# Kernel tuning notes

Hardware: AMD Instinct MI355X
Metric: run time of the kernel (lower is better)

Reference implementation:

```python
import jax, jax.numpy as jnp
import numpy as np
from jax import lax

K = 5          # dynamic kernel size
GROUPS = 8     # inter_channels // group_channels = 128 // 16
R = 2          # pixel shuffle upscale factor
SLOPE = 0.01   # LeakyReLU default negative_slope
EPS = 1e-5     # BatchNorm eps


def conv2d(x, w, b, pad=0):
    # x: [B,C,H,W], w: [O,I,kh,kw]
    y = lax.conv_general_dilated(x, w, (1, 1), [(pad, pad), (pad, pad)],
                                 dimension_numbers=('NCHW', 'OIHW', 'NCHW'))
    return y + b[None, :, None, None]


def pixel_shuffle(x, r):
    B, C, H, W = x.shape
    x = x.reshape(B, C // (r * r), r, r, H, W)
    x = x.transpose(0, 1, 4, 2, 5, 3)  # B, C', H, r, W, r
    return x.reshape(B, C // (r * r), H * r, W * r)


def involution(x, weight, k, groups, pad):
    # x: [B,C,H,W]; weight: [B,groups,k,k,H,W]
    # out[b, g*gc+c, h, w] = sum_ij weight[b,g,i,j,h,w] * x_pad[b, g*gc+c, h+i, w+j]
    B, C, H, W = x.shape
    gc = C // groups
    xp = jnp.pad(x, ((0, 0), (0, 0), (pad, pad), (pad, pad)))
    xg = xp.reshape(B, groups, gc, H + 2 * pad, W + 2 * pad)
    out = jnp.zeros((B, groups, gc, H, W), x.dtype)
    for i in range(k):
        for j in range(k):
            out = out + weight[:, :, None, i, j] * xg[:, :, :, i:i + H, j:j + W]
    return out.reshape(B, C, H, W)


def setup_inputs() -> dict:
    key = jax.random.key(0)
    ks = jax.random.split(key, 16)
    s = 0.05
    return {
        'high_level': jax.random.normal(ks[0], (8, 128, 64, 64), jnp.float32),
        'low_level': jax.random.normal(ks[1], (8, 224, 128, 128), jnp.float32),
        'emb': jax.random.normal(ks[2], (8, 256, 128, 128), jnp.float32),
        'reduce_w': jax.random.normal(ks[3], (128, 256, 1, 1), jnp.float32) * s,
        'reduce_b': jax.random.normal(ks[4], (128,), jnp.float32) * s,
        'conv1_w': jax.random.normal(ks[5], (32, 128, 1, 1), jnp.float32) * s,
        'conv1_b': jax.random.normal(ks[6], (32,), jnp.float32) * s,
        'conv2_w': jax.random.normal(ks[7], (200, 32, 3, 3), jnp.float32) * s,
        'conv2_b': jax.random.normal(ks[8], (200,), jnp.float32) * s,
        'embconv_w': jax.random.normal(ks[9], (32, 256, 1, 1), jnp.float32) * s,
        'embconv_b': jax.random.normal(ks[10], (32,), jnp.float32) * s,
        'out_w': jax.random.normal(ks[11], (64, 128, 1, 1), jnp.float32) * s,
        'out_b': jax.random.normal(ks[12], (64,), jnp.float32) * s,
        'bn_gamma': jnp.ones((64,), jnp.float32),
        'bn_beta': jnp.zeros((64,), jnp.float32),
        'bn_mean': jnp.zeros((64,), jnp.float32),
        'bn_var': jax.random.uniform(ks[13], (64,), jnp.float32, 0.5, 1.5),
    }


def reference(high_level, low_level, emb,
              reduce_w, reduce_b, conv1_w, conv1_b, conv2_w, conv2_b,
              embconv_w, embconv_b, out_w, out_b,
              bn_gamma, bn_beta, bn_mean, bn_var):
    cat = jnp.concatenate([pixel_shuffle(high_level, R), low_level], axis=1)
    cat = conv2d(cat, reduce_w, reduce_b)
    mix = jax.nn.leaky_relu(conv2d(cat, conv1_w, conv1_b)
                            + conv2d(emb, embconv_w, embconv_b), SLOPE)
    w = conv2d(mix, conv2_w, conv2_b, pad=1)  # [B, K*K*GROUPS, H, W]
    B, _, H, W = w.shape
    w = w.reshape(B, GROUPS, K, K, H, W)
    o = involution(cat, w, K, GROUPS, (K - 1) // 2)
    o = conv2d(o, out_w, out_b)
    o = (o - bn_mean[None, :, None, None]) * (bn_gamma[None, :, None, None]
        / jnp.sqrt(bn_var[None, :, None, None] + EPS)) + bn_beta[None, :, None, None]
    return jax.nn.leaky_relu(o, SLOPE)
```

## Files before the change

kernel.cpp:

```cpp
#include <hip/hip_runtime.h>

typedef unsigned short u16; typedef unsigned int u32; typedef unsigned long long u64;
typedef __attribute__((ext_vector_type(8))) short short8;
typedef __attribute__((ext_vector_type(16))) float f32x16;

#define HW 16384

#define RED_B  0
#define C1E_B  128
#define C2_B   160
#define OUT_B  416
#define BN_SC  480
#define BN_SH  544
#define FLAG_OFF   4096
#define RWB_OFF    8192
#define C1B_OFF    73728
#define EMBB_OFF   81920
#define OUTB_OFF   98304
#define C2PB_OFF   114688
#define WEFF_OFF   262144
#define CAT2_OFF   524288
#define MIX_OFF    34078720

__device__ __forceinline__ float bf2f(u16 x){ u32 u=((u32)x)<<16; float f; __builtin_memcpy(&f,&u,4); return f; }
__device__ __forceinline__ u16 f2bf(float f){ u32 u; __builtin_memcpy(&u,&f,4); return (u16)((u + 0x7fffu + ((u>>16)&1u))>>16); }
__device__ __forceinline__ u32 pk2(float a, float b){ return (u32)f2bf(a) | ((u32)f2bf(b)<<16); }
__device__ __forceinline__ float lrelu(float x){ return x>0.f ? x : 0.01f*x; }

template<int M> __device__ __forceinline__ u16 ldb(const void* p, size_t i){
    if (M==1) return ((const u16*)p)[i];
    return f2bf(((const float*)p)[i]);
}
template<int M> __device__ __forceinline__ float ldf(const void* p, size_t i){
    if (M==1) return bf2f(((const u16*)p)[i]);
    return ((const float*)p)[i];
}
__device__ __forceinline__ int swz(int p){ return ((p>>1) ^ (p>>3)) & 7; }

__device__ __forceinline__ void gl16(const void* g, void* l){
    __builtin_amdgcn_global_load_lds(
        (const __attribute__((address_space(1))) u32*)g,
        (__attribute__((address_space(3))) u32*)l, 16, 0, 0);
}

__global__ void detect_kernel(const void* __restrict__ emb, u32* __restrict__ flag){
    int tid = threadIdx.x;
    const u16* p = (const u16*)emb;
    int e = (p[tid*2] >> 7) & 0xFF;
    u64 m = __ballot(e >= 100 && e <= 140);
    if (tid == 0) *flag = (__popcll(m) >= 32) ? 1u : 0u;
}

template<int M>
__device__ __forceinline__ void prep_body(
    const void* rw, const void* rb, const void* c1w, const void* c1b,
    const void* c2w, const void* c2b, const void* ew, const void* eb,
    const void* ow, const void* ob, const void* gam, const void* bet,
    const void* mn, const void* vr, char* ws)
{
    float* wf = (float*)ws;
    int i = blockIdx.x*256 + threadIdx.x;
    if (i < 32768) {
        int o = i>>8, ic = i&255;
        int s = ic>>4, qq = (ic>>3)&1, e = ic&7;
        int dst = (((o>>5)*16 + s)*64 + qq*32 + (o&31))*8 + e;
        ((u16*)(ws+RWB_OFF))[dst] = ldb<M>(rw, i);
    }
    else if (i < 36864)  ((u16*)(ws+C1B_OFF))[i-32768] = ldb<M>(c1w, i-32768);
    else if (i < 45056)  ((u16*)(ws+EMBB_OFF))[i-36864] = ldb<M>(ew, i-36864);
    else if (i < 53248)  ((u16*)(ws+OUTB_OFF))[i-45056] = ldb<M>(ow, i-45056);
    else if (i < 126976) {
        int j = i-53248; int o = j/288, k = j - o*288;
        int tap = k>>5, ic = k&31;
        u16 v = 0;
        if (o < 200) v = ldb<M>(c2w, (size_t)o*288 + ic*9 + tap);
        ((u16*)(ws+C2PB_OFF))[j] = v;
    }
    else if (i < 127584) {
        int j = i-126976;
        if (j < 128) wf[RED_B+j] = ldf<M>(rb, j);
        else if (j < 160) {
            int o = j-128;
            float s = ldf<M>(c1b,o) + ldf<M>(eb,o);
#pragma unroll 8
            for (int ic=0; ic<128; ic++)
                s += ldf<M>(c1w, (size_t)o*128+ic) * ldf<M>(rb, ic);
            wf[C1E_B+o] = s;
        }
        else if (j < 416) { int o = j-160; wf[C2_B+o] = (o<200) ? ldf<M>(c2b,o) : 0.f; }
        else if (j < 480) wf[OUT_B+j-416] = ldf<M>(ob, j-416);
        else if (j < 544) { int c=j-480; wf[BN_SC+c] = ldf<M>(gam,c) * rsqrtf(ldf<M>(vr,c)+1e-5f); }
        else { int c=j-544; wf[BN_SH+c] = ldf<M>(bet,c) - ldf<M>(mn,c)*ldf<M>(gam,c)*rsqrtf(ldf<M>(vr,c)+1e-5f); }
    }
    else if (i < 135776) {
        int j = i - 127584; int oc = j>>8, k2 = j&255;
        float s = 0.f;
#pragma unroll 8
        for (int ic=0; ic<128; ic++)
            s += ldf<M>(c1w, (size_t)oc*128+ic) * ldf<M>(rw, (size_t)ic*256+k2);
        ((u16*)(ws+WEFF_OFF))[oc*256+k2] = f2bf(s);
    }
}

__global__ __launch_bounds__(256) void k_prep(
    const void* rw, const void* rb, const void* c1w, const void* c1b,
    const void* c2w, const void* c2b, const void* ew, const void* eb,
    const void* ow, const void* ob, const void* gam, const void* bet,
    const void* mn, const void* vr, char* ws, const u32* __restrict__ flag)
{
    if (*flag) prep_body<1>(rw,rb,c1w,c1b,c2w,c2b,ew,eb,ow,ob,gam,bet,mn,vr,ws);
    else       prep_body<0>(rw,rb,c1w,c1b,c2w,c2b,ew,eb,ow,ob,gam,bet,mn,vr,ws);
}

__device__ __forceinline__ void trans_half_f32(
    const float* rowbase, int rstart, int po, int jh, u16* At, int chunkIdx)
{
    u32 R2[4][4];
#pragma unroll
    for (int jp=0;jp<4;jp++){
        int r = rstart + 4*jh + jp;
        int v = (r>>2)&15;
        float fa[4], fb[4];
        __builtin_memcpy(fa, rowbase + r*64 + ((2*po)^v)*4, 16);
        __builtin_memcpy(fb, rowbase + r*64 + ((2*po+1)^v)*4, 16);
        R2[jp][0]=pk2(fa[0],fa[1]); R2[jp][1]=pk2(fa[2],fa[3]);
        R2[jp][2]=pk2(fb[0],fb[1]); R2[jp][3]=pk2(fb[2],fb[3]);
    }
#pragma unroll
    for (int p=0;p<8;p++){
        const int u=p>>1, hf=p&1;
        u32 Wh[2];
#pragma unroll
        for (int mp=0;mp<2;mp++){
            u32 A0=R2[2*mp][u], A1=R2[2*mp+1][u];
            Wh[mp] = hf ? ((A0>>16)|(A1&0xffff0000u)) : ((A0&0xffffu)|(A1<<16));
        }
        int pg = 8*po+p;
        __builtin_memcpy(At + pg*264 + ((chunkIdx ^ swz(pg))<<3) + jh*4, Wh, 8);
    }
}

__global__ __launch_bounds__(512) void k_rmf(
    const void* __restrict__ hi, const void* __restrict__ lo, const void* __restrict__ emb,
    const u16* __restrict__ rwB, const u16* __restrict__ weffB, const u16* __restrict__ embB,
    const float* __restrict__ wf, u16* __restrict__ cat2, u16* __restrict__ mixt,
    const u32* __restrict__ flag)
{
    if (*flag != 0u) return;
    __shared__ float rawf[18432];
    __shared__ u16 At[64*264];

    const int tid = threadIdx.x, wvi = tid>>6, lane = tid&63;
    const int col = lane&31, q = lane>>5;
    const int gpx = blockIdx.x*64;
    const int b = gpx>>14, p0 = gpx&16383;
    const int h = p0>>7, w0 = p0&127;

    for (int i=wvi; i<56; i+=8){
        int r = 4*i + (lane>>4);
        int qd = (lane&15) ^ (i&15);
        gl16((const float*)lo + ((size_t)(b*224 + r))*HW + p0 + qd*4,
             (char*)rawf + i*1024);
    }
    for (int i=wvi; i<16; i+=8){
        int hc = 8*i + (lane>>3);
        int qd = (lane&7) ^ (i&7);
        gl16((const float*)hi + ((size_t)(b*128 + hc))*4096 + (size_t)(h>>1)*64 + (w0>>1) + qd*4,
             (char*)rawf + 57344 + i*1024);
    }
    __syncthreads();

    {
        const int co = tid>>4, po = (tid>>1)&7, jh = tid&1;
        if (co >= 4) {
            trans_half_f32(rawf, 8*(co-4), po, jh, At, co);
        } else {
            const int h2 = (h&1)*2;
            u32 E2[4][2], O2[4][2];
#pragma unroll
            for (int jp=0;jp<4;jp++){
                int hc = (8*co + 4*jh + jp)*4 + h2;
                int slot = po ^ ((hc>>3)&7);
                float fe[4], fo[4];
                __builtin_memcpy(fe, rawf + 14336 + hc*32 + slot*4, 16);
                __builtin_memcpy(fo, rawf + 14336 + (hc+1)*32 + slot*4, 16);
                E2[jp][0]=pk2(fe[0],fe[1]); E2[jp][1]=pk2(fe[2],fe[3]);
                O2[jp][0]=pk2(fo[0],fo[1]); O2[jp][1]=pk2(fo[2],fo[3]);
            }
#pragma unroll
            for (int p=0;p<8;p++){
                const int k=p>>1, u=k>>1, hf=k&1;
                u32 Wh[2];
#pragma unroll
                for (int mp=0;mp<2;mp++){
                    u32 A0 = (p&1) ? O2[2*mp][u] : E2[2*mp][u];
                    u32 A1 = (p&1) ? O2[2*mp+1][u] : E2[2*mp+1][u];
                    Wh[mp] = hf ? ((A0>>16)|(A1&0xffff0000u)) : ((A0&0xffffu)|(A1<<16));
                }
                int pg = 8*po+p;
                __builtin_memcpy(At + pg*264 + ((co ^ swz(pg))<<3) + jh*4, Wh, 8);
            }
        }
    }
    __syncthreads();

    for (int i=wvi; i<64; i+=8){
        int r = 4*i + (lane>>4);
        int qd = (lane&15) ^ (i&15);
        gl16((const float*)emb + ((size_t)(b*256 + r))*HW + p0 + qd*4,
             (char*)rawf + i*1024);
    }

    const int pt = wvi>>2, ks = wvi&3;
    const int pp = pt*32 + col, sw = swz(pp);
    const u16* arow = At + pp*264;

    f32x16 racc, macc;
#pragma unroll
    for (int r=0;r<16;r++){ racc[r]=0.f; macc[r]=0.f; }

    short8 Wf[4];
#pragma unroll
    for (int t4=0;t4<4;t4++)
        __builtin_memcpy(&Wf[t4], weffB + (size_t)col*256 + (4*ks+t4)*16 + q*8, 16);

#pragma unroll
    for (int bt=0; bt<4; bt++){
        short8 Bb[4];
#pragma unroll
        for (int si=0;si<4;si++)
            __builtin_memcpy(&Bb[si], rwB + (((size_t)(ks*16 + bt*4 + si))*64 + lane)*8, 16);
#pragma unroll
        for (int si=0;si<4;si++){
            int s = bt*4 + si;
            short8 a; __builtin_memcpy(&a, arow + (((2*s+q)^sw)<<3), 16);
            racc = __builtin_amdgcn_mfma_f32_32x32x16_bf16(a, Bb[si], racc, 0,0,0);
            int d = s - 4*ks;
            if (d>=0 && d<4)
                macc = __builtin_amdgcn_mfma_f32_32x32x16_bf16(a, Wf[d], macc, 0,0,0);
        }
    }
    {
        int oc = ks*32 + col;
        float bias = wf[RED_B + oc];
#pragma unroll
        for (int r=0;r<16;r++){
            int row = (r&3) + 8*(r>>2) + 4*q;
            cat2[((size_t)(gpx + pt*32 + row))*128 + oc] = f2bf(racc[r] + bias);
        }
    }
    __syncthreads();

    {
        const int co = tid>>4, po = (tid>>1)&7, jh = tid&1;
        trans_half_f32(rawf, 8*co, po, jh, At, co);
    }
    __syncthreads();

    {
        short8 Be[4];
#pragma unroll
        for (int t4=0;t4<4;t4++)
            __builtin_memcpy(&Be[t4], embB + (size_t)col*256 + (4*ks+t4)*16 + q*8, 16);
#pragma unroll
        for (int t4=0;t4<4;t4++){
            int t = 4*ks + t4;
            short8 a; __builtin_memcpy(&a, arow + (((2*t+q)^sw)<<3), 16);
            macc = __builtin_amdgcn_mfma_f32_32x32x16_bf16(a, Be[t4], macc, 0,0,0);
        }
    }

    float* exch = rawf;
    if (ks != 0){
#pragma unroll
        for (int r=0;r<16;r++){
            int row = (r&3) + 8*(r>>2) + 4*q;
            exch[pt*3072 + (ks-1)*1024 + row*32 + col] = macc[r];
        }
    }
    __syncthreads();
    if (ks == 0){
        float bias = wf[C1E_B + col];
#pragma unroll
        for (int r=0;r<16;r++){
            int row = (r&3) + 8*(r>>2) + 4*q;
            int base = pt*3072 + row*32 + col;
            float v = macc[r] + exch[base] + exch[base+1024] + exch[base+2048] + bias;
            mixt[((size_t)(gpx + pt*32 + row))*32 + col] = f2bf(lrelu(v));
        }
    }
}

__global__ __launch_bounds__(512) void k_rm(
    const void* __restrict__ hi, const void* __restrict__ lo, const void* __restrict__ emb,
    const u16* __restrict__ rwB, const u16* __restrict__ weffB, const u16* __restrict__ embB,
    const float* __restrict__ wf, u16* __restrict__ cat2, u16* __restrict__ mixt,
    const u32* __restrict__ flag)
{
    if (*flag != 1u) return;
    __shared__ u16 At1[64*264];
    __shared__ u16 At2[64*264];
    __shared__ u16 raw[34816];

    const int tid = threadIdx.x, wvi = tid>>6, lane = tid&63;
    const int col = lane&31, q = lane>>5;
    const int gpx = blockIdx.x*64;
    const int b = gpx>>14, p0 = gpx&16383;
    const int h = p0>>7, w0 = p0&127;

    {
        for (int i=wvi; i<28; i+=8){
            int chunk = i*64 + lane;
            int ch = chunk>>3, p8 = chunk&7;
            gl16((const u16*)lo + ((size_t)(b*224+ch))*HW + p0 + p8*8,
                 (char*)raw + i*1024);
        }
        {
            int i = wvi;
            int chunk = i*64 + lane;
            int hc = chunk>>2, c4 = chunk&3;
            gl16((const u16*)hi + ((size_t)(b*128+hc))*4096 + (size_t)(h>>1)*64 + (w0>>1) + c4*8,
                 (char*)raw + 28672 + i*1024);
        }
        for (int i=wvi; i<32; i+=8){
            int chunk = i*64 + lane;
            int ch = chunk>>3, p8 = chunk&7;
            gl16((const u16*)emb + ((size_t)(b*256+ch))*HW + p0 + p8*8,
                 (char*)raw + 36864 + i*1024);
        }
    }
    __syncthreads();

    {
        const int sthr = tid & 255;
        const int co = sthr>>3, po = sthr&7;
        u32 W[8][4];
        if (tid >= 256) {
            u32 R[8][4];
#pragma unroll
            for (int j=0;j<8;j++)
                __builtin_memcpy(&R[j][0], raw + 18432 + (8*co+j)*64 + po*8, 16);
#pragma unroll
            for (int p=0;p<8;p++){
                const int u = p>>1, hf = p&1;
#pragma unroll
                for (int m=0;m<4;m++){
                    u32 A0 = R[2*m][u], A1 = R[2*m+1][u];
                    W[p][m] = hf ? ((A0>>16) | (A1 & 0xffff0000u))
                                 : ((A0 & 0xffffu) | (A1<<16));
                }
            }
#pragma unroll
            for (int p=0;p<8;p++){
                int pg = 8*po + p;
                __builtin_memcpy(At2 + pg*264 + ((co ^ swz(pg))<<3), &W[p][0], 16);
            }
        } else if (co >= 4) {
            u32 R[8][4];
#pragma unroll
            for (int j=0;j<8;j++)
                __builtin_memcpy(&R[j][0], raw + (8*(co-4)+j)*64 + po*8, 16);
#pragma unroll
            for (int p=0;p<8;p++){
                const int u = p>>1, hf = p&1;
#pragma unroll
                for (int m=0;m<4;m++){
                    u32 A0 = R[2*m][u], A1 = R[2*m+1][u];
                    W[p][m] = hf ? ((A0>>16) | (A1 & 0xffff0000u))
                                 : ((A0 & 0xffffu) | (A1<<16));
                }
            }
#pragma unroll
            for (int p=0;p<8;p++){
                int pg = 8*po + p;
                __builtin_memcpy(At1 + pg*264 + ((co ^ swz(pg))<<3), &W[p][0], 16);
            }
        } else {
            const int h2 = (h&1)*2;
            u32 E[8][2], O[8][2];
#pragma unroll
            for (int j=0;j<8;j++){
                int hc = (8*co+j)*4 + h2;
                __builtin_memcpy(&E[j][0], raw + 14336 + hc*32 + po*4, 8);
                __builtin_memcpy(&O[j][0], raw + 14336 + (hc+1)*32 + po*4, 8);
            }
#pragma unroll
            for (int p=0;p<8;p++){
                const int k = p>>1, u = k>>1, hf = k&1;
#pragma unroll
                for (int m=0;m<4;m++){
                    u32 A0, A1;
                    if (p&1){ A0 = O[2*m][u]; A1 = O[2*m+1][u]; }
                    else    { A0 = E[2*m][u]; A1 = E[2*m+1][u]; }
                    W[p][m] = hf ? ((A0>>16) | (A1 & 0xffff0000u))
                                 : ((A0 & 0xffffu) | (A1<<16));
                }
            }
#pragma unroll
            for (int p=0;p<8;p++){
                int pg = 8*po + p;
                __builtin_memcpy(At1 + pg*264 + ((co ^ swz(pg))<<3), &W[p][0], 16);
            }
        }
    }
    __syncthreads();

    const int pt = wvi>>2, ks = wvi&3;
    const int pp = pt*32 + col, sw = swz(pp);
    const u16* arow1 = At1 + pp*264;
    const u16* arow2 = At2 + pp*264;

    f32x16 racc, macc;
#pragma unroll
    for (int r=0;r<16;r++){ racc[r]=0.f; macc[r]=0.f; }

    short8 Wf[4], Be2[4];
#pragma unroll
    for (int t4=0;t4<4;t4++)
        __builtin_memcpy(&Wf[t4], weffB + (size_t)col*256 + (4*ks+t4)*16 + q*8, 16);
#pragma unroll
    for (int t4=0;t4<4;t4++)
        __builtin_memcpy(&Be2[t4], embB + (size_t)col*256 + (4*ks+t4)*16 + q*8, 16);

#pragma unroll
    for (int bt=0; bt<4; bt++){
        short8 Bb[4];
#pragma unroll
        for (int si=0;si<4;si++)
            __builtin_memcpy(&Bb[si], rwB + (((size_t)(ks*16 + bt*4 + si))*64 + lane)*8, 16);
#pragma unroll
        for (int si=0;si<4;si++){
            int s = bt*4 + si;
            short8 a; __builtin_memcpy(&a, arow1 + (((2*s+q)^sw)<<3), 16);
            racc = __builtin_amdgcn_mfma_f32_32x32x16_bf16(a, Bb[si], racc, 0,0,0);
            int d = s - 4*ks;
            if (d>=0 && d<4)
                macc = __builtin_amdgcn_mfma_f32_32x32x16_bf16(a, Wf[d], macc, 0,0,0);
        }
    }
#pragma unroll
    for (int t4=0;t4<4;t4++){
        int t = 4*ks + t4;
        short8 a; __builtin_memcpy(&a, arow2 + (((2*t+q)^sw)<<3), 16);
        macc = __builtin_amdgcn_mfma_f32_32x32x16_bf16(a, Be2[t4], macc, 0,0,0);
    }
    {
        int oc = ks*32 + col;
        float bias = wf[RED_B + oc];
#pragma unroll
        for (int r=0;r<16;r++){
            int row = (r&3) + 8*(r>>2) + 4*q;
            cat2[((size_t)(gpx + pt*32 + row))*128 + oc] = f2bf(racc[r] + bias);
        }
    }

    float* exch = (float*)raw;
    if (ks != 0){
#pragma unroll
        for (int r=0;r<16;r++){
            int row = (r&3) + 8*(r>>2) + 4*q;
            exch[pt*3072 + (ks-1)*1024 + row*32 + col] = macc[r];
        }
    }
    __syncthreads();
    if (ks == 0){
        float bias = wf[C1E_B + col];
#pragma unroll
        for (int r=0;r<16;r++){
            int row = (r&3) + 8*(r>>2) + 4*q;
            int base = pt*3072 + row*32 + col;
            float v = macc[r] + exch[base] + exch[base+1024] + exch[base+2048] + bias;
            mixt[((size_t)(gpx + pt*32 + row))*32 + col] = f2bf(lrelu(v));
        }
    }
}

template<int M>
__device__ __forceinline__ void inv_body(
    const u16* __restrict__ cat2, const u16* __restrict__ mixt,
    const u16* __restrict__ c2B, const u16* __restrict__ outB,
    const float* __restrict__ wf, void* __restrict__ out,
    u16* halo_m, u16* wgt_l, u16* halo_c, u16* og)
{
    const int tid = threadIdx.x, wvi = tid>>6, lane = tid&63;
    const int col = lane&31, q = lane>>5;
    const int b = blockIdx.y, ty = blockIdx.x>>3, tx = blockIdx.x&7;
    const int py = tid>>4, px = tid&15;

    f32x16 acc[2][2];
#pragma unroll
    for (int i=0;i<2;i++)
#pragma unroll
    for (int j=0;j<2;j++)
#pragma unroll
    for (int r=0;r<16;r++) acc[i][j][r] = 0.f;

#pragma unroll
    for (int i=0;i<6;i++){
        int idx = tid + i*256;
        if (idx < 1296){
            int point = idx>>2, cq = idx&3;
            int y = ty*16 + point/18 - 1, x = tx*16 + point%18 - 1;
            short8 v;
            if (y>=0 && y<128 && x>=0 && x<128)
                __builtin_memcpy(&v, mixt + ((size_t)(b*HW + y*128 + x))*32 + cq*8, 16);
            else { short z=0; v = (short8){z,z,z,z,z,z,z,z}; }
            *(short8*)(halo_m + point*40 + cq*8) = v;
        }
    }
    __syncthreads();

#pragma unroll 1
    for (int g=0; g<8; g++){
        __syncthreads();

        const int o = g*25 + col;
        short8 Bf[18];
#pragma unroll
        for (int s=0;s<18;s++)
            __builtin_memcpy(&Bf[s], c2B + (size_t)o*288 + s*16 + q*8, 16);

#pragma unroll
        for (int i=0;i<4;i++){
            int idx = tid + i*256;
            if (idx < 800){
                int point = idx>>1, cq = idx&1;
                int y = ty*16 + point/20 - 2, x = tx*16 + point%20 - 2;
                short8 v;
                if (y>=0 && y<128 && x>=0 && x<128)
                    __builtin_memcpy(&v, cat2 + ((size_t)(b*HW + y*128 + x))*128 + g*16 + cq*8, 16);
                else { short z=0; v = (short8){z,z,z,z,z,z,z,z}; }
                *(short8*)(halo_c + point*16 + cq*8) = v;
            }
        }

        f32x16 c0, c1;
#pragma unroll
        for (int r=0;r<16;r++){ c0[r]=0.f; c1[r]=0.f; }
        const int p0 = wvi*64 + col, p1 = p0 + 32;
        const int pya = p0>>4, pxa = p0&15, pyb = p1>>4, pxb = p1&15;
#pragma unroll
        for (int s=0;s<18;s++){
            int tap = s>>1, ih = s&1;
            int dy = tap/3, dx = tap%3;
            short8 a0, a1;
            __builtin_memcpy(&a0, halo_m + ((pya+dy)*18 + pxa+dx)*40 + ih*16 + q*8, 16);
            __builtin_memcpy(&a1, halo_m + ((pyb+dy)*18 + pxb+dx)*40 + ih*16 + q*8, 16);
            c0 = __builtin_amdgcn_mfma_f32_32x32x16_bf16(a0, Bf[s], c0, 0,0,0);
            c1 = __builtin_amdgcn_mfma_f32_32x32x16_bf16(a1, Bf[s], c1, 0,0,0);
        }
        {
            float bias = wf[C2_B + o];
#pragma unroll
            for (int rt2=0; rt2<2; rt2++){
                int mb = wvi*64 + rt2*32;
#pragma unroll
                for (int r=0;r<16;r+=2){
                    int row0 = (r&3) + 8*(r>>2) + 4*q;
                    float v0 = (rt2 ? c1[r]   : c0[r])   + bias;
                    float v1 = (rt2 ? c1[r+1] : c0[r+1]) + bias;
                    u32 pkv = (u32)f2bf(v0) | ((u32)f2bf(v1)<<16);
                    *(u32*)(wgt_l + (size_t)col*264 + mb + row0) = pkv;
                }
            }
        }
        __syncthreads();

        float wvv[25];
#pragma unroll
        for (int t=0;t<25;t++) wvv[t] = bf2f(wgt_l[t*264 + tid]);

        float a16[16];
#pragma unroll
        for (int cc=0;cc<16;cc++) a16[cc]=0.f;
#pragma unroll
        for (int t=0;t<25;t++){
            int dy = t/5, dx = t%5;
            u32 vv[8];
            __builtin_memcpy(vv, halo_c + ((py+dy)*20 + px+dx)*16, 32);
            float wt = wvv[t];
#pragma unroll
            for (int r=0;r<8;r++){
                u32 u = vv[r];
                u32 ulo = u<<16, uhi = u & 0xffff0000u;
                float x0, x1;
                __builtin_memcpy(&x0,&ulo,4); __builtin_memcpy(&x1,&uhi,4);
                a16[2*r]   += wt*x0;
                a16[2*r+1] += wt*x1;
            }
        }
        u32 pk[8];
#pragma unroll
        for (int r=0;r<8;r++) pk[r] = (u32)f2bf(a16[2*r]) | ((u32)f2bf(a16[2*r+1])<<16);
        __builtin_memcpy(og + tid*16, pk, 32);
        __syncthreads();

        short8 bo0, bo1;
        __builtin_memcpy(&bo0, outB + (size_t)(col)*128      + g*16 + q*8, 16);
        __builtin_memcpy(&bo1, outB + (size_t)(32+col)*128   + g*16 + q*8, 16);
#pragma unroll
        for (int rt2=0; rt2<2; rt2++){
            int prow = (wvi*2 + rt2)*32 + col;
            short8 a; __builtin_memcpy(&a, og + prow*16 + q*8, 16);
            acc[rt2][0] = __builtin_amdgcn_mfma_f32_32x32x16_bf16(a, bo0, acc[rt2][0], 0,0,0);
            acc[rt2][1] = __builtin_amdgcn_mfma_f32_32x32x16_bf16(a, bo1, acc[rt2][1], 0,0,0);
        }
    }
#pragma unroll
    for (int rt2=0; rt2<2; rt2++)
#pragma unroll
    for (int nt=0; nt<2; nt++){
        int oc = nt*32 + col;
        float bias = wf[OUT_B+oc], sc = wf[BN_SC+oc], sh = wf[BN_SH+oc];
#pragma unroll
        for (int r=0;r<16;r++){
            int row = (r&3) + 8*(r>>2) + 4*q;
            int p = (wvi*2 + rt2)*32 + row;
            int yy = ty*16 + (p>>4), xx = tx*16 + (p&15);
            float v = lrelu((acc[rt2][nt][r] + bias)*sc + sh);
            size_t oidx = ((size_t)(b*64 + oc))*HW + yy*128 + xx;
            if (M==1) ((u16*)out)[oidx] = f2bf(v);
            else ((float*)out)[oidx] = v;
        }
    }
}

__global__ __launch_bounds__(256,2) void k_inv(
    const u16* __restrict__ cat2, const u16* __restrict__ mixt,
    const u16* __restrict__ c2B, const u16* __restrict__ outB,
    const float* __restrict__ wf, void* __restrict__ out, const u32* __restrict__ flag)
{
    __shared__ u16 halo_m[324*40];
    __shared__ u16 wgt_l[32*264];
    __shared__ u16 halo_c[400*16];
    __shared__ u16 og[256*16];
    if (*flag) inv_body<1>(cat2, mixt, c2B, outB, wf, out, halo_m, wgt_l, halo_c, og);
    else       inv_body<0>(cat2, mixt, c2B, outB, wf, out, halo_m, wgt_l, halo_c, og);
}

extern "C" void kernel_launch(void* const* d_in, const int* in_sizes, int n_in,
                              void* d_out, int out_size, void* d_ws, size_t ws_size,
                              hipStream_t stream) {
    const void* hi  = d_in[0];
    const void* lo  = d_in[1];
    const void* emb = d_in[2];
    char* ws = (char*)d_ws;
    float* wf = (float*)ws;
    u32* flag = (u32*)(ws + FLAG_OFF);
    u16* cat2 = (u16*)(ws + CAT2_OFF);
    u16* mixt = (u16*)(ws + MIX_OFF);

    detect_kernel<<<1, 64, 0, stream>>>(emb, flag);

    k_prep<<<531,256,0,stream>>>(d_in[3],d_in[4],d_in[5],d_in[6],d_in[7],d_in[8],
        d_in[9],d_in[10],d_in[11],d_in[12],d_in[13],d_in[14],d_in[15],d_in[16], ws, flag);

    k_rmf<<<2048,512,0,stream>>>(hi, lo, emb, (const u16*)(ws+RWB_OFF),
                                 (const u16*)(ws+WEFF_OFF), (const u16*)(ws+EMBB_OFF),
                                 wf, cat2, mixt, flag);
    k_rm<<<2048,512,0,stream>>>(hi, lo, emb, (const u16*)(ws+RWB_OFF),
                                (const u16*)(ws+WEFF_OFF), (const u16*)(ws+EMBB_OFF),
                                wf, cat2, mixt, flag);

    k_inv<<<dim3(64,8),256,0,stream>>>(cat2, mixt, (const u16*)(ws+C2PB_OFF),
                                       (const u16*)(ws+OUTB_OFF), wf, d_out, flag);
}
```

Before: 428.8 us.

## Split raw f32 staging into halves to shrink LDS and raise occupancy

The k_rmf kernel used to stage all of low_level (plus high_level) and then all of emb in a 72KB shared buffer. It now stages these in two phases through a 40KB buffer, transposing each half into the bf16 A tile before loading the next half. The emb MFMA work is split across the two phases by k-slice. A new transq_f32 helper is used for the transpose, with one quarter of the work per thread. The smaller LDS footprint should allow more resident blocks per CU, at the cost of extra __syncthreads and serialized load/transpose phases.

```diff
diff --git a/kernel.cpp b/kernel.cpp
--- a/kernel.cpp
+++ b/kernel.cpp
@@ -43,6 +43,25 @@
         (__attribute__((address_space(3))) u32*)l, 16, 0, 0);
 }
 
+__device__ __forceinline__ void transq_f32(
+    const float* rawb, int ibuf, int rlo, int v, int po, u16* dst, int atChunk, int jq)
+{
+    const float* base = rawb + ibuf*256 + rlo*64;
+    float fa[4], fb[4], ga[4], gb[4];
+    int qa = ((2*po)^v)*4, qb = ((2*po+1)^v)*4;
+    __builtin_memcpy(fa, base + qa, 16);
+    __builtin_memcpy(fb, base + qb, 16);
+    __builtin_memcpy(ga, base + 64 + qa, 16);
+    __builtin_memcpy(gb, base + 64 + qb, 16);
+#pragma unroll
+    for (int p=0;p<8;p++){
+        float x0 = (p<4) ? fa[p] : fb[p-4];
+        float x1 = (p<4) ? ga[p] : gb[p-4];
+        int pg = 8*po + p;
+        *(u32*)(dst + pg*264 + ((atChunk ^ swz(pg))<<3) + jq*2) = pk2(x0, x1);
+    }
+}
+
 __global__ void detect_kernel(const void* __restrict__ emb, u32* __restrict__ flag){
     int tid = threadIdx.x;
     const u16* p = (const u16*)emb;
@@ -112,34 +131,6 @@
     else       prep_body<0>(rw,rb,c1w,c1b,c2w,c2b,ew,eb,ow,ob,gam,bet,mn,vr,ws);
 }
 
-__device__ __forceinline__ void trans_half_f32(
-    const float* rowbase, int rstart, int po, int jh, u16* At, int chunkIdx)
-{
-    u32 R2[4][4];
-#pragma unroll
-    for (int jp=0;jp<4;jp++){
-        int r = rstart + 4*jh + jp;
-        int v = (r>>2)&15;
-        float fa[4], fb[4];
-        __builtin_memcpy(fa, rowbase + r*64 + ((2*po)^v)*4, 16);
-        __builtin_memcpy(fb, rowbase + r*64 + ((2*po+1)^v)*4, 16);
-        R2[jp][0]=pk2(fa[0],fa[1]); R2[jp][1]=pk2(fa[2],fa[3]);
-        R2[jp][2]=pk2(fb[0],fb[1]); R2[jp][3]=pk2(fb[2],fb[3]);
-    }
-#pragma unroll
-    for (int p=0;p<8;p++){
-        const int u=p>>1, hf=p&1;
-        u32 Wh[2];
-#pragma unroll
-        for (int mp=0;mp<2;mp++){
-            u32 A0=R2[2*mp][u], A1=R2[2*mp+1][u];
-            Wh[mp] = hf ? ((A0>>16)|(A1&0xffff0000u)) : ((A0&0xffffu)|(A1<<16));
-        }
-        int pg = 8*po+p;
-        __builtin_memcpy(At + pg*264 + ((chunkIdx ^ swz(pg))<<3) + jh*4, Wh, 8);
-    }
-}
-
 __global__ __launch_bounds__(512) void k_rmf(
     const void* __restrict__ hi, const void* __restrict__ lo, const void* __restrict__ emb,
     const u16* __restrict__ rwB, const u16* __restrict__ weffB, const u16* __restrict__ embB,
@@ -147,71 +138,81 @@
     const u32* __restrict__ flag)
 {
     if (*flag != 0u) return;
-    __shared__ float rawf[18432];
-    __shared__ u16 At[64*264];
+    __shared__ char ldsb[40960 + 64*264*2];
+    float* rawf = (float*)ldsb;
+    u16* At = (u16*)(ldsb + 40960);
 
     const int tid = threadIdx.x, wvi = tid>>6, lane = tid&63;
     const int col = lane&31, q = lane>>5;
     const int gpx = blockIdx.x*64;
     const int b = gpx>>14, p0 = gpx&16383;
     const int h = p0>>7, w0 = p0&127;
-
-    for (int i=wvi; i<56; i+=8){
+    const int pt = wvi>>2, ks = wvi&3;
+
+    for (int i=wvi; i<32; i+=8){
         int r = 4*i + (lane>>4);
         int qd = (lane&15) ^ (i&15);
-        gl16((const float*)lo + ((size_t)(b*224 + r))*HW + p0 + qd*4,
-             (char*)rawf + i*1024);
-    }
-    for (int i=wvi; i<16; i+=8){
-        int hc = 8*i + (lane>>3);
-        int qd = (lane&7) ^ (i&7);
+        gl16((const float*)lo + ((size_t)(b*224 + r))*HW + p0 + qd*4, (char*)rawf + i*1024);
+    }
+    __syncthreads();
+
+    {
+        const int c = tid>>5, po = (tid>>2)&7, jq = tid&3;
+        int r = 8*c + 2*jq;
+        transq_f32(rawf, r>>2, r&3, (r>>2)&15, po, At, 4+c, jq);
+    }
+    __syncthreads();
+
+    for (int idx=wvi; idx<24; idx+=8){
+        int ig = 32 + idx;
+        int r = 4*ig + (lane>>4);
+        int qd = (lane&15) ^ (ig&15);
+        gl16((const float*)lo + ((size_t)(b*224 + r))*HW + p0 + qd*4, (char*)rawf + idx*1024);
+    }
+    for (int idx=wvi; idx<16; idx+=8){
+        int hc = 8*idx + (lane>>3);
+        int qd = (lane&7) ^ (idx&7);
         gl16((const float*)hi + ((size_t)(b*128 + hc))*4096 + (size_t)(h>>1)*64 + (w0>>1) + qd*4,
-             (char*)rawf + 57344 + i*1024);
-    }
-    __syncthreads();
-
-    {
-        const int co = tid>>4, po = (tid>>1)&7, jh = tid&1;
-        if (co >= 4) {
-            trans_half_f32(rawf, 8*(co-4), po, jh, At, co);
-        } else {
-            const int h2 = (h&1)*2;
-            u32 E2[4][2], O2[4][2];
-#pragma unroll
-            for (int jp=0;jp<4;jp++){
-                int hc = (8*co + 4*jh + jp)*4 + h2;
-                int slot = po ^ ((hc>>3)&7);
-                float fe[4], fo[4];
-                __builtin_memcpy(fe, rawf + 14336 + hc*32 + slot*4, 16);
-                __builtin_memcpy(fo, rawf + 14336 + (hc+1)*32 + slot*4, 16);
-                E2[jp][0]=pk2(fe[0],fe[1]); E2[jp][1]=pk2(fe[2],fe[3]);
-                O2[jp][0]=pk2(fo[0],fo[1]); O2[jp][1]=pk2(fo[2],fo[3]);
-            }
-#pragma unroll
-            for (int p=0;p<8;p++){
-                const int k=p>>1, u=k>>1, hf=k&1;
-                u32 Wh[2];
-#pragma unroll
-                for (int mp=0;mp<2;mp++){
-                    u32 A0 = (p&1) ? O2[2*mp][u] : E2[2*mp][u];
-                    u32 A1 = (p&1) ? O2[2*mp+1][u] : E2[2*mp+1][u];
-                    Wh[mp] = hf ? ((A0>>16)|(A1&0xffff0000u)) : ((A0&0xffffu)|(A1<<16));
-                }
-                int pg = 8*po+p;
-                __builtin_memcpy(At + pg*264 + ((co ^ swz(pg))<<3) + jh*4, Wh, 8);
-            }
-        }
-    }
-    __syncthreads();
-
-    for (int i=wvi; i<64; i+=8){
+             (char*)rawf + (24+idx)*1024);
+    }
+    __syncthreads();
+
+    if (tid < 384){
+        const int c = tid>>5, po = (tid>>2)&7, jq = tid&3;
+        int rg = 128 + 8*c + 2*jq;
+        int ig = rg>>2;
+        transq_f32(rawf, ig-32, rg&3, ig&15, po, At, 20+c, jq);
+    } else {
+        const int u = tid-384, co = u>>5, po = (u>>2)&7, jj = u&3;
+        const int h2 = (h&1)*2;
+        const float* hbase = rawf + 6144;
+        float fe0[4], fo0[4], fe1[4], fo1[4];
+        {
+            int hcA = (8*co + 2*jj)*4 + h2;
+            int hcB = (8*co + 2*jj + 1)*4 + h2;
+            int sA = po ^ ((hcA>>3)&7);
+            int sB = po ^ ((hcB>>3)&7);
+            __builtin_memcpy(fe0, hbase + hcA*32 + sA*4, 16);
+            __builtin_memcpy(fo0, hbase + (hcA+1)*32 + sA*4, 16);
+            __builtin_memcpy(fe1, hbase + hcB*32 + sB*4, 16);
+            __builtin_memcpy(fo1, hbase + (hcB+1)*32 + sB*4, 16);
+        }
+#pragma unroll
+        for (int p=0;p<8;p++){
+            float x0 = (p&1) ? fo0[p>>1] : fe0[p>>1];
+            float x1 = (p&1) ? fo1[p>>1] : fe1[p>>1];
+            int pg = 8*po + p;
+            *(u32*)(At + pg*264 + ((co ^ swz(pg))<<3) + jj*2) = pk2(x0, x1);
+        }
+    }
+    __syncthreads();
+
+    for (int i=wvi; i<32; i+=8){
         int r = 4*i + (lane>>4);
         int qd = (lane&15) ^ (i&15);
-        gl16((const float*)emb + ((size_t)(b*256 + r))*HW + p0 + qd*4,
-             (char*)rawf + i*1024);
-    }
-
-    const int pt = wvi>>2, ks = wvi&3;
+        gl16((const float*)emb + ((size_t)(b*256 + r))*HW + p0 + qd*4, (char*)rawf + i*1024);
+    }
+
     const int pp = pt*32 + col, sw = swz(pp);
     const u16* arow = At + pp*264;
 
@@ -252,12 +253,42 @@
     __syncthreads();
 
     {
-        const int co = tid>>4, po = (tid>>1)&7, jh = tid&1;
-        trans_half_f32(rawf, 8*co, po, jh, At, co);
+        const int c = tid>>5, po = (tid>>2)&7, jq = tid&3;
+        int r = 8*c + 2*jq;
+        transq_f32(rawf, r>>2, r&3, (r>>2)&15, po, At, c, jq);
+    }
+    __syncthreads();
+
+    for (int idx=wvi; idx<32; idx+=8){
+        int ig = 32 + idx;
+        int r = 4*ig + (lane>>4);
+        int qd = (lane&15) ^ (ig&15);
+        gl16((const float*)emb + ((size_t)(b*256 + r))*HW + p0 + qd*4, (char*)rawf + idx*1024);
+    }
+
+    if (ks < 2){
+        short8 Be[4];
+#pragma unroll
+        for (int t4=0;t4<4;t4++)
+            __builtin_memcpy(&Be[t4], embB + (size_t)col*256 + (4*ks+t4)*16 + q*8, 16);
+#pragma unroll
+        for (int t4=0;t4<4;t4++){
+            int t = 4*ks + t4;
+            short8 a; __builtin_memcpy(&a, arow + (((2*t+q)^sw)<<3), 16);
+            macc = __builtin_amdgcn_mfma_f32_32x32x16_bf16(a, Be[t4], macc, 0,0,0);
+        }
     }
     __syncthreads();
 
     {
+        const int c = tid>>5, po = (tid>>2)&7, jq = tid&3;
+        int rg = 128 + 8*c + 2*jq;
+        int ig = rg>>2;
+        transq_f32(rawf, ig-32, rg&3, ig&15, po, At, 16+c, jq);
+    }
+    __syncthreads();
+
+    if (ks >= 2){
         short8 Be[4];
 #pragma unroll
         for (int t4=0;t4<4;t4++)
```

Result: faster. 417.8 us (-2.6%).
